# Performance work log

Measured on AMD Instinct MI355X. Metric: run time of the kernel, lower is better.

## Reference

```python
import jax, jax.numpy as jnp
import numpy as np

D = 768        # LaBSE_DIM
N = 64         # neighborhood size (center at index 0)
BS = 512
N_HEAD = 1
GAT_NUM = 2
NEG_SLOPE = 0.2
EPS = 1e-12


def setup_inputs() -> dict:
    key = jax.random.key(0)
    k_feat, k_adj, kw, ks, kd, kmw = jax.random.split(key, 6)
    feats = jax.random.normal(k_feat, (BS, N, D), dtype=jnp.float32)
    adj = (jax.random.uniform(k_adj, (BS, N, N)) < 0.125).astype(jnp.float32)
    batch = jnp.concatenate([feats, adj], axis=-1)  # [bs, n, D+n]
    # xavier_uniform for w [h, f_in, f_out]: bound = sqrt(6/(f_in+f_out))
    bw = float(np.sqrt(6.0 / (D + D)))
    w = jax.random.uniform(kw, (N_HEAD, D, D), minval=-bw, maxval=bw, dtype=jnp.float32)
    ba = float(np.sqrt(6.0 / (D + 1)))
    a_src = jax.random.uniform(ks, (N_HEAD, D, 1), minval=-ba, maxval=ba, dtype=jnp.float32)
    a_dst = jax.random.uniform(kd, (N_HEAD, D, 1), minval=-ba, maxval=ba, dtype=jnp.float32)
    gat_bias = jnp.zeros((D,), dtype=jnp.float32)
    bm = float(np.sqrt(1.0 / (2 * D)))  # torch Linear default init bound
    kmw1, kmb = jax.random.split(kmw)
    mlp_w = jax.random.uniform(kmw1, (D, 2 * D), minval=-bm, maxval=bm, dtype=jnp.float32)
    mlp_b = jax.random.uniform(kmb, (D,), minval=-bm, maxval=bm, dtype=jnp.float32)
    return {"batch": batch, "w": w, "a_src": a_src, "a_dst": a_dst,
            "gat_bias": gat_bias, "mlp_w": mlp_w, "mlp_b": mlp_b}


def _l2norm(x):
    # F.normalize(p=2, dim=1): divide by max(||x||, eps)
    n = jnp.sqrt(jnp.sum(x * x, axis=1, keepdims=True))
    return x / jnp.maximum(n, EPS)


def _gat(h, allowed, w, a_src, a_dst, bias):
    # h: [bs, n, D]; allowed: [bs, 1, n, n] bool (adj | eye)
    hp = jnp.einsum('bnf,hfo->bhno', h, w)                  # [bs, H, n, D]
    th = jnp.tanh(hp)
    src = jnp.einsum('bhno,hop->bhnp', th, a_src)           # [bs, H, n, 1]
    dst = jnp.einsum('bhno,hop->bhnp', th, a_dst)           # [bs, H, n, 1]
    attn = src + jnp.swapaxes(dst, -1, -2)                  # [bs, H, n, n]
    attn = jnp.where(attn >= 0, attn, NEG_SLOPE * attn)     # leaky_relu(0.2)
    attn = jnp.where(allowed, attn, -jnp.inf)
    attn = jax.nn.softmax(attn, axis=-1)                    # dropout off (eval)
    out = jnp.einsum('bhnm,bhmo->bhno', attn, hp) + bias
    return out[:, 0]                                        # squeeze(1), n_head == 1


def reference(batch, w, a_src, a_dst, gat_bias, mlp_w, mlp_b):
    x = batch[:, :, :D]                                     # [bs, n, D]
    adj = batch[:, :, D:] != 0                              # [bs, n, n] bool
    eye = jnp.eye(N, dtype=bool)
    allowed = (adj | eye)[:, None]                          # [bs, 1, n, n]
    center = x[:, 0]
    h = x
    for _ in range(GAT_NUM):
        h = _gat(h, allowed, w, a_src, a_dst, gat_bias)
    center_neigh = _l2norm(h[:, 0])                         # neighbor_norm
    out = jnp.concatenate([center, center_neigh], axis=1) @ mlp_w.T + mlp_b
    out = _l2norm(out)                                      # emb_norm
    return out
```

## Files before the change

kernel.cpp:

```cpp
#include <hip/hip_runtime.h>
#include <math.h>

#define DF 768
#define NN 64
#define DN 832
#define LDH 776
#define LDT 72
#define LDA2 388
#define NEG_SLOPE 0.2f

typedef _Float16 f16;
typedef __attribute__((ext_vector_type(4))) _Float16 f16x4;
typedef __attribute__((ext_vector_type(8))) _Float16 f16x8;
typedef __attribute__((ext_vector_type(4))) float f32x4;

__device__ __forceinline__ float tanh_fast(float x) {
  return 1.0f - 2.0f / (__expf(2.0f * x) + 1.0f);
}

__global__ __launch_bounds__(64) void prep_frag(
    const float* __restrict__ w,
    const float* __restrict__ mw,
    f16* __restrict__ wTf,
    f16* __restrict__ mwf)
{
  const int bid  = blockIdx.x;
  const int lane = threadIdx.x;
  const int l16  = lane & 15;
  const int quad = lane >> 4;
  if (bid < 48 * 24) {
    const int ot = bid / 24, ks = bid % 24;
    const int o = ot * 16 + l16;
    f16 tmp[8];
#pragma unroll
    for (int j = 0; j < 8; ++j) {
      int k = ks * 32 + quad * 8 + j;
      tmp[j] = (f16)w[(size_t)k * DF + o];
    }
    *(f16x8*)&wTf[((size_t)bid * 64 + lane) * 8] = *(f16x8*)tmp;
  } else {
    const int b2 = bid - 48 * 24;
    const int ot = b2 / 48, ks = b2 % 48;
    const int o = ot * 16 + l16;
    const float* src = &mw[(size_t)o * (2 * DF) + ks * 32 + quad * 8];
    float4 v0 = *(const float4*)src;
    float4 v1 = *(const float4*)(src + 4);
    f16x8 h = {(f16)v0.x, (f16)v0.y, (f16)v0.z, (f16)v0.w,
               (f16)v1.x, (f16)v1.y, (f16)v1.z, (f16)v1.w};
    *(f16x8*)&mwf[((size_t)b2 * 64 + lane) * 8] = h;
  }
}

__global__ __launch_bounds__(1024, 4) void gat_fused(
    const float* __restrict__ batch,
    const f16* __restrict__ wTf,
    const float* __restrict__ a_src,
    const float* __restrict__ a_dst,
    const float* __restrict__ gat_bias,
    f16* __restrict__ cneighW)
{
  __shared__ __align__(16) f16 Hbuf[DF * LDT];
  __shared__ __align__(16) f16 attnB[NN * LDT];
  __shared__ float asrcL[DF], adstL[DF], biasL[DF];
  __shared__ float srcv[NN], dstv[NN];
  __shared__ float redS[16 * NN], redD[16 * NN];
  __shared__ unsigned long long maskRow[NN];
  __shared__ float attn0[NN];
  __shared__ float h2row[DF];
  __shared__ float ssqred[16];

  const int tid  = threadIdx.x;
  const int lane = tid & 63;
  const int wv   = tid >> 6;
  const int l16  = lane & 15;
  const int quad = lane >> 4;
  const int b    = blockIdx.x;
  const int cb   = wv * 48;

  const float* bb = batch + (size_t)b * (NN * DN);

  for (int i = tid; i < DF; i += 1024) {
    asrcL[i] = a_src[i];
    adstL[i] = a_dst[i];
    biasL[i] = gat_bias[i];
  }
  for (int i = tid; i < NN * (DF / 4); i += 1024) {
    int r = i / (DF / 4), c4 = i - r * (DF / 4);
    float4 v = *(const float4*)&bb[r * DN + c4 * 4];
    f16x4 h4 = {(f16)v.x, (f16)v.y, (f16)v.z, (f16)v.w};
    *(f16x4*)&Hbuf[r * LDH + c4 * 4] = h4;
  }
#pragma unroll
  for (int r = 0; r < 4; ++r) {
    int n = wv * 4 + r;
    float av = bb[n * DN + DF + lane];
    unsigned long long m = __ballot(av != 0.0f);
    if (lane == 0) maskRow[n] = m | (1ULL << n);
  }
  __syncthreads();

  const f16* wp0 = wTf + (size_t)(wv * 3) * 24 * 512 + lane * 8;

  for (int layer = 0; layer < 2; ++layer) {
    f32x4 acc[4][3];
#pragma unroll
    for (int rt = 0; rt < 4; ++rt)
#pragma unroll
      for (int ct = 0; ct < 3; ++ct)
        acc[rt][ct] = (f32x4){0.f, 0.f, 0.f, 0.f};

    f16x8 bfr[3], bnx[3];
#pragma unroll
    for (int ct = 0; ct < 3; ++ct)
      bfr[ct] = *(const f16x8*)(wp0 + ct * 12288);

#pragma clang loop unroll(disable)
    for (int k0 = 0; k0 < DF; k0 += 32) {
      int ksn = (k0 + 32 < DF) ? ((k0 + 32) >> 5) : 0;
#pragma unroll
      for (int ct = 0; ct < 3; ++ct)
        bnx[ct] = *(const f16x8*)(wp0 + ct * 12288 + ksn * 512);
      f16x8 af[4];
#pragma unroll
      for (int rt = 0; rt < 4; ++rt)
        af[rt] = *(const f16x8*)&Hbuf[(rt * 16 + l16) * LDH + k0 + quad * 8];
#pragma unroll
      for (int rt = 0; rt < 4; ++rt)
#pragma unroll
        for (int ct = 0; ct < 3; ++ct)
          acc[rt][ct] = __builtin_amdgcn_mfma_f32_16x16x32_f16(af[rt], bfr[ct], acc[rt][ct], 0, 0, 0);
#pragma unroll
      for (int ct = 0; ct < 3; ++ct) bfr[ct] = bnx[ct];
    }
    __syncthreads();

#pragma unroll
    for (int rt = 0; rt < 4; ++rt)
#pragma unroll
      for (int ct = 0; ct < 3; ++ct) {
        int row0 = rt * 16 + quad * 4;
        int col  = cb + ct * 16 + l16;
        f16x4 h4 = {(f16)acc[rt][ct][0], (f16)acc[rt][ct][1],
                    (f16)acc[rt][ct][2], (f16)acc[rt][ct][3]};
        *(f16x4*)&Hbuf[col * LDT + row0] = h4;
      }
    __syncthreads();

    {
      float s = 0.f, d = 0.f;
      int m = lane;
      int o0 = wv * 48;
      for (int o = o0; o < o0 + 48; ++o) {
        float t = tanh_fast((float)Hbuf[o * LDT + m]);
        s += t * asrcL[o];
        d += t * adstL[o];
      }
      redS[wv * 64 + m] = s;
      redD[wv * 64 + m] = d;
    }
    __syncthreads();
    if (tid < 64) {
      float s = 0.f, d = 0.f;
#pragma unroll
      for (int q = 0; q < 16; ++q) { s += redS[q * 64 + tid]; d += redD[q * 64 + tid]; }
      srcv[tid] = s;
      dstv[tid] = d;
    }
    __syncthreads();

    if (layer == 0) {
#pragma unroll
      for (int r = 0; r < 4; ++r) {
        int n = wv * 4 + r;
        float logit = srcv[n] + dstv[lane];
        logit = logit >= 0.f ? logit : NEG_SLOPE * logit;
        bool ok = (maskRow[n] >> lane) & 1ULL;
        float v = ok ? logit : -1e30f;
        float mx = v;
#pragma unroll
        for (int off = 32; off > 0; off >>= 1) mx = fmaxf(mx, __shfl_xor(mx, off, 64));
        float e = ok ? __expf(v - mx) : 0.f;
        float sm = e;
#pragma unroll
        for (int off = 32; off > 0; off >>= 1) sm += __shfl_xor(sm, off, 64);
        attnB[n * LDT + lane] = (f16)(e / sm);
      }
      __syncthreads();

      f32x4 acc2[4][3];
#pragma unroll
      for (int rt = 0; rt < 4; ++rt)
#pragma unroll
        for (int ct = 0; ct < 3; ++ct)
          acc2[rt][ct] = (f32x4){0.f, 0.f, 0.f, 0.f};
#pragma unroll
      for (int k0 = 0; k0 < NN; k0 += 32) {
        f16x8 af2[4];
#pragma unroll
        for (int rt = 0; rt < 4; ++rt)
          af2[rt] = *(const f16x8*)&attnB[(rt * 16 + l16) * LDT + k0 + quad * 8];
#pragma unroll
        for (int ct = 0; ct < 3; ++ct) {
          f16x8 bf = *(const f16x8*)&Hbuf[(cb + ct * 16 + l16) * LDT + k0 + quad * 8];
#pragma unroll
          for (int rt = 0; rt < 4; ++rt)
            acc2[rt][ct] = __builtin_amdgcn_mfma_f32_16x16x32_f16(af2[rt], bf, acc2[rt][ct], 0, 0, 0);
        }
      }
      __syncthreads();
#pragma unroll
      for (int rt = 0; rt < 4; ++rt)
#pragma unroll
        for (int ct = 0; ct < 3; ++ct)
#pragma unroll
          for (int i = 0; i < 4; ++i) {
            int row = rt * 16 + quad * 4 + i;
            int col = cb + ct * 16 + l16;
            Hbuf[row * LDH + col] = (f16)(acc2[rt][ct][i] + biasL[col]);
          }
      __syncthreads();
    } else {
      if (wv == 0) {
        float logit = srcv[0] + dstv[lane];
        logit = logit >= 0.f ? logit : NEG_SLOPE * logit;
        bool ok = (maskRow[0] >> lane) & 1ULL;
        float v = ok ? logit : -1e30f;
        float mx = v;
#pragma unroll
        for (int off = 32; off > 0; off >>= 1) mx = fmaxf(mx, __shfl_xor(mx, off, 64));
        float e = ok ? __expf(v - mx) : 0.f;
        float sm = e;
#pragma unroll
        for (int off = 32; off > 0; off >>= 1) sm += __shfl_xor(sm, off, 64);
        attn0[lane] = e / sm;
      }
      __syncthreads();
      if (tid < DF) {
        const int o = tid;
        const f16* rowp = &Hbuf[o * LDT];
        float a = biasL[o];
#pragma unroll
        for (int j = 0; j < 8; ++j) {
          f16x8 v = *(const f16x8*)&rowp[j * 8];
#pragma unroll
          for (int e = 0; e < 8; ++e) a += attn0[j * 8 + e] * (float)v[e];
        }
        h2row[o] = a;
      }
      __syncthreads();
      float p = (tid < DF) ? h2row[tid] * h2row[tid] : 0.f;
#pragma unroll
      for (int off = 32; off > 0; off >>= 1) p += __shfl_xor(p, off, 64);
      if (lane == 0) ssqred[wv] = p;
      __syncthreads();
      if (tid == 0) {
        float ss = 0.f;
#pragma unroll
        for (int q = 0; q < 16; ++q) ss += ssqred[q];
        ssqred[0] = 1.0f / fmaxf(sqrtf(ss), 1e-12f);
      }
      __syncthreads();
      float scale = ssqred[0];
      if (tid < DF)
        cneighW[(size_t)b * DF + tid] = (f16)(h2row[tid] * scale);
    }
  }
}

__global__ __launch_bounds__(256) void final_mlp(
    const float* __restrict__ batch,
    const f16* __restrict__ cneighW,
    const f16* __restrict__ mwf,
    float* __restrict__ partial)
{
  __shared__ __align__(16) f16 Abuf[16 * LDA2];
  const int tid  = threadIdx.x;
  const int lane = tid & 63;
  const int wv   = tid >> 6;
  const int l16  = lane & 15;
  const int quad = lane >> 4;
  const int b0   = blockIdx.x * 16;
  const int cb   = blockIdx.y * 128 + wv * 32;
  const int zc   = blockIdx.z;

  const f16* mpf = mwf + ((size_t)(blockIdx.y * 8 + wv * 2) * 48 + zc * 12) * 512 + lane * 8;
  f16x8 bfr[2], bnx[2];
  bfr[0] = *(const f16x8*)(mpf);
  bfr[1] = *(const f16x8*)(mpf + 24576);

  for (int i = tid; i < 16 * 96; i += 256) {
    int r = i / 96, c4 = i - r * 96;
    int j = zc * 384 + c4 * 4;
    f16x4 h4;
    if (j < DF) {
      float4 v = *(const float4*)&batch[(size_t)(b0 + r) * (NN * DN) + j];
      h4 = (f16x4){(f16)v.x, (f16)v.y, (f16)v.z, (f16)v.w};
    } else {
      h4 = *(const f16x4*)&cneighW[(size_t)(b0 + r) * DF + (j - DF)];
    }
    *(f16x4*)&Abuf[r * LDA2 + c4 * 4] = h4;
  }
  __syncthreads();

  f32x4 acc[2];
  acc[0] = (f32x4){0.f, 0.f, 0.f, 0.f};
  acc[1] = (f32x4){0.f, 0.f, 0.f, 0.f};

#pragma clang loop unroll(disable)
  for (int k0 = 0; k0 < 384; k0 += 32) {
    int ksn = (k0 + 32 < 384) ? ((k0 + 32) >> 5) : 0;
    bnx[0] = *(const f16x8*)(mpf + ksn * 512);
    bnx[1] = *(const f16x8*)(mpf + 24576 + ksn * 512);
    f16x4 a0 = *(const f16x4*)&Abuf[l16 * LDA2 + k0 + quad * 8];
    f16x4 a1 = *(const f16x4*)&Abuf[l16 * LDA2 + k0 + quad * 8 + 4];
    f16x8 af = {a0[0], a0[1], a0[2], a0[3], a1[0], a1[1], a1[2], a1[3]};
    acc[0] = __builtin_amdgcn_mfma_f32_16x16x32_f16(af, bfr[0], acc[0], 0, 0, 0);
    acc[1] = __builtin_amdgcn_mfma_f32_16x16x32_f16(af, bfr[1], acc[1], 0, 0, 0);
    bfr[0] = bnx[0];
    bfr[1] = bnx[1];
  }

#pragma unroll
  for (int ct = 0; ct < 2; ++ct) {
    int col = cb + ct * 16 + l16;
#pragma unroll
    for (int i = 0; i < 4; ++i) {
      int row = quad * 4 + i;
      partial[((size_t)zc * 512 + b0 + row) * DF + col] = acc[ct][i];
    }
  }
}

__global__ __launch_bounds__(256) void l2norm_rows(
    const float* __restrict__ partial,
    const float* __restrict__ mlp_b,
    float* __restrict__ out)
{
  const int lane = threadIdx.x & 63;
  const int wv   = threadIdx.x >> 6;
  const int row  = blockIdx.x * 4 + wv;
  float v[12];
  float ss = 0.f;
#pragma unroll
  for (int j = 0; j < 12; ++j) {
    int col = j * 64 + lane;
    float s = partial[((size_t)0 * 512 + row) * DF + col]
            + partial[((size_t)1 * 512 + row) * DF + col]
            + partial[((size_t)2 * 512 + row) * DF + col]
            + partial[((size_t)3 * 512 + row) * DF + col]
            + mlp_b[col];
    v[j] = s;
    ss += s * s;
  }
#pragma unroll
  for (int off = 32; off > 0; off >>= 1) ss += __shfl_xor(ss, off, 64);
  float sc = 1.0f / fmaxf(sqrtf(ss), 1e-12f);
  float* rp = out + (size_t)row * DF;
#pragma unroll
  for (int j = 0; j < 12; ++j) rp[j * 64 + lane] = v[j] * sc;
}

extern "C" void kernel_launch(void* const* d_in, const int* in_sizes, int n_in,
                              void* d_out, int out_size, void* d_ws, size_t ws_size,
                              hipStream_t stream) {
  const float* batch    = (const float*)d_in[0];
  const float* w        = (const float*)d_in[1];
  const float* a_src    = (const float*)d_in[2];
  const float* a_dst    = (const float*)d_in[3];
  const float* gat_bias = (const float*)d_in[4];
  const float* mlp_w    = (const float*)d_in[5];
  const float* mlp_b    = (const float*)d_in[6];
  float* out = (float*)d_out;

  f16* wTf     = (f16*)d_ws;
  f16* mwf     = wTf + (size_t)DF * DF;
  f16* cneighW = mwf + (size_t)DF * 2 * DF;
  float* partial = (float*)(cneighW + (size_t)512 * DF);

  prep_frag<<<dim3(48 * 24 + 48 * 48), dim3(64), 0, stream>>>(w, mlp_w, wTf, mwf);
  gat_fused<<<dim3(512), dim3(1024), 0, stream>>>(batch, wTf, a_src, a_dst, gat_bias, cneighW);
  final_mlp<<<dim3(32, 6, 4), dim3(256), 0, stream>>>(batch, cneighW, mwf, partial);
  l2norm_rows<<<dim3(128), dim3(256), 0, stream>>>(partial, mlp_b, out);
}
```

Before: 292.5 us.

## Make GAT blocks persistent over two batch items and keep W fragments in registers

The GAT kernel now launches 256 blocks, and each block processes two batch items in turn. Each wave loads its whole slice of the transformed W matrix (3x24 f16x8 fragments) into registers once and reuses it for both layers of both items, so the per-k-step global loads of W disappear. The first pass streams W in with a two-step prefetch. The register array is very large for a 1024-thread block with limited VGPRs per thread, which risks heavy scratch spilling and fewer blocks running in parallel.

```diff
diff --git a/kernel.cpp b/kernel.cpp
--- a/kernel.cpp
+++ b/kernel.cpp
@@ -74,195 +74,216 @@
   const int wv   = tid >> 6;
   const int l16  = lane & 15;
   const int quad = lane >> 4;
-  const int b    = blockIdx.x;
   const int cb   = wv * 48;
 
-  const float* bb = batch + (size_t)b * (NN * DN);
+  const f16* wp0 = wTf + (size_t)(wv * 3) * 24 * 512 + lane * 8;
+
+  f16x8 Breg[3][24];
+#pragma unroll
+  for (int ct = 0; ct < 3; ++ct) {
+    Breg[ct][0] = *(const f16x8*)(wp0 + ct * 12288);
+    Breg[ct][1] = *(const f16x8*)(wp0 + ct * 12288 + 512);
+  }
 
   for (int i = tid; i < DF; i += 1024) {
     asrcL[i] = a_src[i];
     adstL[i] = a_dst[i];
     biasL[i] = gat_bias[i];
   }
-  for (int i = tid; i < NN * (DF / 4); i += 1024) {
-    int r = i / (DF / 4), c4 = i - r * (DF / 4);
-    float4 v = *(const float4*)&bb[r * DN + c4 * 4];
-    f16x4 h4 = {(f16)v.x, (f16)v.y, (f16)v.z, (f16)v.w};
-    *(f16x4*)&Hbuf[r * LDH + c4 * 4] = h4;
-  }
-#pragma unroll
-  for (int r = 0; r < 4; ++r) {
-    int n = wv * 4 + r;
-    float av = bb[n * DN + DF + lane];
-    unsigned long long m = __ballot(av != 0.0f);
-    if (lane == 0) maskRow[n] = m | (1ULL << n);
-  }
-  __syncthreads();
-
-  const f16* wp0 = wTf + (size_t)(wv * 3) * 24 * 512 + lane * 8;
-
-  for (int layer = 0; layer < 2; ++layer) {
-    f32x4 acc[4][3];
-#pragma unroll
-    for (int rt = 0; rt < 4; ++rt)
-#pragma unroll
-      for (int ct = 0; ct < 3; ++ct)
-        acc[rt][ct] = (f32x4){0.f, 0.f, 0.f, 0.f};
-
-    f16x8 bfr[3], bnx[3];
-#pragma unroll
-    for (int ct = 0; ct < 3; ++ct)
-      bfr[ct] = *(const f16x8*)(wp0 + ct * 12288);
-
-#pragma clang loop unroll(disable)
-    for (int k0 = 0; k0 < DF; k0 += 32) {
-      int ksn = (k0 + 32 < DF) ? ((k0 + 32) >> 5) : 0;
-#pragma unroll
-      for (int ct = 0; ct < 3; ++ct)
-        bnx[ct] = *(const f16x8*)(wp0 + ct * 12288 + ksn * 512);
-      f16x8 af[4];
+
+  for (int item = 0; item < 2; ++item) {
+    const int b = blockIdx.x + item * 256;
+    const float* bb = batch + (size_t)b * (NN * DN);
+
+    __syncthreads();
+
+    for (int i = tid; i < NN * (DF / 4); i += 1024) {
+      int r = i / (DF / 4), c4 = i - r * (DF / 4);
+      float4 v = *(const float4*)&bb[r * DN + c4 * 4];
+      f16x4 h4 = {(f16)v.x, (f16)v.y, (f16)v.z, (f16)v.w};
+      *(f16x4*)&Hbuf[r * LDH + c4 * 4] = h4;
+    }
+#pragma unroll
+    for (int r = 0; r < 4; ++r) {
+      int n = wv * 4 + r;
+      float av = bb[n * DN + DF + lane];
+      unsigned long long m = __ballot(av != 0.0f);
+      if (lane == 0) maskRow[n] = m | (1ULL << n);
+    }
+    __syncthreads();
+
+    for (int layer = 0; layer < 2; ++layer) {
+      f32x4 acc[4][3];
 #pragma unroll
       for (int rt = 0; rt < 4; ++rt)
-        af[rt] = *(const f16x8*)&Hbuf[(rt * 16 + l16) * LDH + k0 + quad * 8];
-#pragma unroll
-      for (int rt = 0; rt < 4; ++rt)
 #pragma unroll
         for (int ct = 0; ct < 3; ++ct)
-          acc[rt][ct] = __builtin_amdgcn_mfma_f32_16x16x32_f16(af[rt], bfr[ct], acc[rt][ct], 0, 0, 0);
-#pragma unroll
-      for (int ct = 0; ct < 3; ++ct) bfr[ct] = bnx[ct];
-    }
-    __syncthreads();
-
-#pragma unroll
-    for (int rt = 0; rt < 4; ++rt)
-#pragma unroll
-      for (int ct = 0; ct < 3; ++ct) {
-        int row0 = rt * 16 + quad * 4;
-        int col  = cb + ct * 16 + l16;
-        f16x4 h4 = {(f16)acc[rt][ct][0], (f16)acc[rt][ct][1],
-                    (f16)acc[rt][ct][2], (f16)acc[rt][ct][3]};
-        *(f16x4*)&Hbuf[col * LDT + row0] = h4;
-      }
-    __syncthreads();
-
-    {
-      float s = 0.f, d = 0.f;
-      int m = lane;
-      int o0 = wv * 48;
-      for (int o = o0; o < o0 + 48; ++o) {
-        float t = tanh_fast((float)Hbuf[o * LDT + m]);
-        s += t * asrcL[o];
-        d += t * adstL[o];
-      }
-      redS[wv * 64 + m] = s;
-      redD[wv * 64 + m] = d;
-    }
-    __syncthreads();
-    if (tid < 64) {
-      float s = 0.f, d = 0.f;
-#pragma unroll
-      for (int q = 0; q < 16; ++q) { s += redS[q * 64 + tid]; d += redD[q * 64 + tid]; }
-      srcv[tid] = s;
-      dstv[tid] = d;
-    }
-    __syncthreads();
-
-    if (layer == 0) {
-#pragma unroll
-      for (int r = 0; r < 4; ++r) {
-        int n = wv * 4 + r;
-        float logit = srcv[n] + dstv[lane];
-        logit = logit >= 0.f ? logit : NEG_SLOPE * logit;
-        bool ok = (maskRow[n] >> lane) & 1ULL;
-        float v = ok ? logit : -1e30f;
-        float mx = v;
-#pragma unroll
-        for (int off = 32; off > 0; off >>= 1) mx = fmaxf(mx, __shfl_xor(mx, off, 64));
-        float e = ok ? __expf(v - mx) : 0.f;
-        float sm = e;
-#pragma unroll
-        for (int off = 32; off > 0; off >>= 1) sm += __shfl_xor(sm, off, 64);
-        attnB[n * LDT + lane] = (f16)(e / sm);
+          acc[rt][ct] = (f32x4){0.f, 0.f, 0.f, 0.f};
+
+      if (item == 0 && layer == 0) {
+#pragma unroll
+        for (int ks = 0; ks < 24; ++ks) {
+          if (ks < 22) {
+#pragma unroll
+            for (int ct = 0; ct < 3; ++ct)
+              Breg[ct][ks + 2] = *(const f16x8*)(wp0 + ct * 12288 + (ks + 2) * 512);
+          }
+          f16x8 af[4];
+#pragma unroll
+          for (int rt = 0; rt < 4; ++rt)
+            af[rt] = *(const f16x8*)&Hbuf[(rt * 16 + l16) * LDH + ks * 32 + quad * 8];
+#pragma unroll
+          for (int rt = 0; rt < 4; ++rt)
+#pragma unroll
+            for (int ct = 0; ct < 3; ++ct)
+              acc[rt][ct] = __builtin_amdgcn_mfma_f32_16x16x32_f16(af[rt], Breg[ct][ks], acc[rt][ct], 0, 0, 0);
+        }
+      } else {
+#pragma unroll
+        for (int ks = 0; ks < 24; ++ks) {
+          f16x8 af[4];
+#pragma unroll
+          for (int rt = 0; rt < 4; ++rt)
+            af[rt] = *(const f16x8*)&Hbuf[(rt * 16 + l16) * LDH + ks * 32 + quad * 8];
+#pragma unroll
+          for (int rt = 0; rt < 4; ++rt)
+#pragma unroll
+            for (int ct = 0; ct < 3; ++ct)
+              acc[rt][ct] = __builtin_amdgcn_mfma_f32_16x16x32_f16(af[rt], Breg[ct][ks], acc[rt][ct], 0, 0, 0);
+        }
       }
       __syncthreads();
 
-      f32x4 acc2[4][3];
 #pragma unroll
       for (int rt = 0; rt < 4; ++rt)
 #pragma unroll
-        for (int ct = 0; ct < 3; ++ct)
-          acc2[rt][ct] = (f32x4){0.f, 0.f, 0.f, 0.f};
-#pragma unroll
-      for (int k0 = 0; k0 < NN; k0 += 32) {
-        f16x8 af2[4];
-#pragma unroll
-        for (int rt = 0; rt < 4; ++rt)
-          af2[rt] = *(const f16x8*)&attnB[(rt * 16 + l16) * LDT + k0 + quad * 8];
-#pragma unroll
         for (int ct = 0; ct < 3; ++ct) {
-          f16x8 bf = *(const f16x8*)&Hbuf[(cb + ct * 16 + l16) * LDT + k0 + quad * 8];
-#pragma unroll
-          for (int rt = 0; rt < 4; ++rt)
-            acc2[rt][ct] = __builtin_amdgcn_mfma_f32_16x16x32_f16(af2[rt], bf, acc2[rt][ct], 0, 0, 0);
-        }
+          int row0 = rt * 16 + quad * 4;
+          int col  = cb + ct * 16 + l16;
+          f16x4 h4 = {(f16)acc[rt][ct][0], (f16)acc[rt][ct][1],
+                      (f16)acc[rt][ct][2], (f16)acc[rt][ct][3]};
+          *(f16x4*)&Hbuf[col * LDT + row0] = h4;
+        }
+      __syncthreads();
+
+      {
+        float s = 0.f, d = 0.f;
+        int m = lane;
+        int o0 = wv * 48;
+        for (int o = o0; o < o0 + 48; ++o) {
+          float t = tanh_fast((float)Hbuf[o * LDT + m]);
+          s += t * asrcL[o];
+          d += t * adstL[o];
+        }
+        redS[wv * 64 + m] = s;
+        redD[wv * 64 + m] = d;
       }
       __syncthreads();
-#pragma unroll
-      for (int rt = 0; rt < 4; ++rt)
-#pragma unroll
-        for (int ct = 0; ct < 3; ++ct)
-#pragma unroll
-          for (int i = 0; i < 4; ++i) {
-            int row = rt * 16 + quad * 4 + i;
-            int col = cb + ct * 16 + l16;
-            Hbuf[row * LDH + col] = (f16)(acc2[rt][ct][i] + biasL[col]);
-          }
-      __syncthreads();
-    } else {
-      if (wv == 0) {
-        float logit = srcv[0] + dstv[lane];
-        logit = logit >= 0.f ? logit : NEG_SLOPE * logit;
-        bool ok = (maskRow[0] >> lane) & 1ULL;
-        float v = ok ? logit : -1e30f;
-        float mx = v;
-#pragma unroll
-        for (int off = 32; off > 0; off >>= 1) mx = fmaxf(mx, __shfl_xor(mx, off, 64));
-        float e = ok ? __expf(v - mx) : 0.f;
-        float sm = e;
-#pragma unroll
-        for (int off = 32; off > 0; off >>= 1) sm += __shfl_xor(sm, off, 64);
-        attn0[lane] = e / sm;
+      if (tid < 64) {
+        float s = 0.f, d = 0.f;
+#pragma unroll
+        for (int q = 0; q < 16; ++q) { s += redS[q * 64 + tid]; d += redD[q * 64 + tid]; }
+        srcv[tid] = s;
+        dstv[tid] = d;
       }
       __syncthreads();
-      if (tid < DF) {
-        const int o = tid;
-        const f16* rowp = &Hbuf[o * LDT];
-        float a = biasL[o];
-#pragma unroll
-        for (int j = 0; j < 8; ++j) {
-          f16x8 v = *(const f16x8*)&rowp[j * 8];
-#pragma unroll
-          for (int e = 0; e < 8; ++e) a += attn0[j * 8 + e] * (float)v[e];
-        }
-        h2row[o] = a;
+
+      if (layer == 0) {
+#pragma unroll
+        for (int r = 0; r < 4; ++r) {
+          int n = wv * 4 + r;
+          float logit = srcv[n] + dstv[lane];
+          logit = logit >= 0.f ? logit : NEG_SLOPE * logit;
+          bool ok = (maskRow[n] >> lane) & 1ULL;
+          float v = ok ? logit : -1e30f;
+          float mx = v;
+#pragma unroll
+          for (int off = 32; off > 0; off >>= 1) mx = fmaxf(mx, __shfl_xor(mx, off, 64));
+          float e = ok ? __expf(v - mx) : 0.f;
+          float sm = e;
+#pragma unroll
+          for (int off = 32; off > 0; off >>= 1) sm += __shfl_xor(sm, off, 64);
+          attnB[n * LDT + lane] = (f16)(e / sm);
+        }
+        __syncthreads();
+
+        f32x4 acc2[4][3];
+#pragma unroll
+        for (int rt = 0; rt < 4; ++rt)
+#pragma unroll
+          for (int ct = 0; ct < 3; ++ct)
+            acc2[rt][ct] = (f32x4){0.f, 0.f, 0.f, 0.f};
+#pragma unroll
+        for (int k0 = 0; k0 < NN; k0 += 32) {
+          f16x8 af2[4];
+#pragma unroll
+          for (int rt = 0; rt < 4; ++rt)
+            af2[rt] = *(const f16x8*)&attnB[(rt * 16 + l16) * LDT + k0 + quad * 8];
+#pragma unroll
+          for (int ct = 0; ct < 3; ++ct) {
+            f16x8 bf = *(const f16x8*)&Hbuf[(cb + ct * 16 + l16) * LDT + k0 + quad * 8];
+#pragma unroll
+            for (int rt = 0; rt < 4; ++rt)
+              acc2[rt][ct] = __builtin_amdgcn_mfma_f32_16x16x32_f16(af2[rt], bf, acc2[rt][ct], 0, 0, 0);
+          }
+        }
+        __syncthreads();
+#pragma unroll
+        for (int rt = 0; rt < 4; ++rt)
+#pragma unroll
+          for (int ct = 0; ct < 3; ++ct)
+#pragma unroll
+            for (int i = 0; i < 4; ++i) {
+              int row = rt * 16 + quad * 4 + i;
+              int col = cb + ct * 16 + l16;
+              Hbuf[row * LDH + col] = (f16)(acc2[rt][ct][i] + biasL[col]);
+            }
+        __syncthreads();
+      } else {
+        if (wv == 0) {
+          float logit = srcv[0] + dstv[lane];
+          logit = logit >= 0.f ? logit : NEG_SLOPE * logit;
+          bool ok = (maskRow[0] >> lane) & 1ULL;
+          float v = ok ? logit : -1e30f;
+          float mx = v;
+#pragma unroll
+          for (int off = 32; off > 0; off >>= 1) mx = fmaxf(mx, __shfl_xor(mx, off, 64));
+          float e = ok ? __expf(v - mx) : 0.f;
+          float sm = e;
+#pragma unroll
+          for (int off = 32; off > 0; off >>= 1) sm += __shfl_xor(sm, off, 64);
+          attn0[lane] = e / sm;
+        }
+        __syncthreads();
+        if (tid < DF) {
+          const int o = tid;
+          const f16* rowp = &Hbuf[o * LDT];
+          float a = biasL[o];
+#pragma unroll
+          for (int j = 0; j < 8; ++j) {
+            f16x8 v = *(const f16x8*)&rowp[j * 8];
+#pragma unroll
+            for (int e = 0; e < 8; ++e) a += attn0[j * 8 + e] * (float)v[e];
+          }
+          h2row[o] = a;
+        }
+        __syncthreads();
+        float p = (tid < DF) ? h2row[tid] * h2row[tid] : 0.f;
+#pragma unroll
+        for (int off = 32; off > 0; off >>= 1) p += __shfl_xor(p, off, 64);
+        if (lane == 0) ssqred[wv] = p;
+        __syncthreads();
+        if (tid == 0) {
+          float ss = 0.f;
+#pragma unroll
+          for (int q = 0; q < 16; ++q) ss += ssqred[q];
+          ssqred[0] = 1.0f / fmaxf(sqrtf(ss), 1e-12f);
+        }
+        __syncthreads();
+        float scale = ssqred[0];
+        if (tid < DF)
+          cneighW[(size_t)b * DF + tid] = (f16)(h2row[tid] * scale);
       }
-      __syncthreads();
-      float p = (tid < DF) ? h2row[tid] * h2row[tid] : 0.f;
-#pragma unroll
-      for (int off = 32; off > 0; off >>= 1) p += __shfl_xor(p, off, 64);
-      if (lane == 0) ssqred[wv] = p;
-      __syncthreads();
-      if (tid == 0) {
-        float ss = 0.f;
-#pragma unroll
-        for (int q = 0; q < 16; ++q) ss += ssqred[q];
-        ssqred[0] = 1.0f / fmaxf(sqrtf(ss), 1e-12f);
-      }
-      __syncthreads();
-      float scale = ssqred[0];
-      if (tid < DF)
-        cneighW[(size_t)b * DF + tid] = (f16)(h2row[tid] * scale);
     }
   }
 }
@@ -378,7 +399,7 @@
   float* partial = (float*)(cneighW + (size_t)512 * DF);
 
   prep_frag<<<dim3(48 * 24 + 48 * 48), dim3(64), 0, stream>>>(w, mlp_w, wTf, mwf);
-  gat_fused<<<dim3(512), dim3(1024), 0, stream>>>(batch, wTf, a_src, a_dst, gat_bias, cneighW);
+  gat_fused<<<dim3(256), dim3(1024), 0, stream>>>(batch, wTf, a_src, a_dst, gat_bias, cneighW);
   final_mlp<<<dim3(32, 6, 4), dim3(256), 0, stream>>>(batch, cneighW, mwf, partial);
   l2norm_rows<<<dim3(128), dim3(256), 0, stream>>>(partial, mlp_b, out);
 }
```

Measured after the change: 565.5 us. +93.3%, slower.
